# Kernel tuning notes

Hardware: AMD Instinct MI355X
Metric: run time of the kernel (lower is better)

The kernel has to match this reference:

```python
import jax, jax.numpy as jnp
import numpy as np

# Dims: img=64, Nslice=16, Ncoil=4, Nsingular=4, Necho=3, N_readout=32, Npoint=96
IMG = 64
NSLICE = 16
NCOIL = 4
NSING = 4
NECHO = 3
NRO = 32
NPT = 96


def setup_inputs() -> dict:
    key = jax.random.key(0)
    k = jax.random.split(key, 6)
    singulars = jax.random.normal(k[0], (IMG, IMG, NSLICE, NSING, NECHO, 2), jnp.float32)
    smap = jax.random.normal(k[1], (NCOIL, IMG, IMG, NSLICE, 2), jnp.float32)
    # k-space trajectory in radians, [-pi, pi)
    ktraj = (jax.random.uniform(k[2], (1, NRO, NPT, 2), jnp.float32) - 0.5) * (2.0 * np.pi)
    Ur_list = jax.random.normal(k[3], (1, NRO, NSING), jnp.float32)
    slice_bin_list = jax.random.randint(k[4], (NRO,), 0, NSLICE)
    dc = jax.random.uniform(k[5], (NPT,), jnp.float32)
    return {"singulars": singulars, "smap": smap, "ktraj": ktraj,
            "Ur_list": Ur_list, "slice_bin_list": slice_bin_list, "dc": dc}


def reference(singulars, smap, ktraj, Ur_list, slice_bin_list, dc):
    # dc is density compensation; used only in the original (custom) backward.
    X, Y, Z, Ns, Ne, _ = singulars.shape
    C = smap.shape[0]
    sc = singulars[..., 0] + 1j * singulars[..., 1]              # [X,Y,Z,Ns,Ne] c64
    sc = jnp.transpose(sc, (3, 4, 0, 1, 2)).reshape(Ns * Ne, 1, X, Y, Z)  # [S,1,X,Y,Z]
    # sign flip on odd slices (fftshift trick along kz)
    sign = jnp.where(jnp.arange(Z) % 2 == 1, -1.0, 1.0).astype(jnp.float32)
    sc = sc * sign
    sm = smap[..., 0] + 1j * smap[..., 1]                        # [C,X,Y,Z]
    sc = sc * sm[None]                                            # [S,C,X,Y,Z]
    scf = jnp.fft.fft(sc, axis=-1)                                # FFT along slice dim

    kt = ktraj[0]                                                 # [R,P,2]
    ur = Ur_list[0]                                               # [R,Ns]
    # gather the slice image for each readout
    img_g = scf[..., slice_bin_list]                              # [S,C,X,Y,R]

    xs = (jnp.arange(X) - X // 2).astype(jnp.float32)
    ys = (jnp.arange(Y) - Y // 2).astype(jnp.float32)
    # exact (type-2) NUFFT, separable phase: exp(-i(w0*x + w1*y)), centered grid
    ex = jnp.exp(-1j * kt[..., 0, None] * xs)                     # [R,P,X]
    ey = jnp.exp(-1j * kt[..., 1, None] * ys)                     # [R,P,Y]
    t1 = jnp.einsum('scxyr,rpx->scrpy', img_g, ex)                # [S,C,R,P,Y]
    nuf = jnp.einsum('scrpy,rpy->scrp', t1, ey)                   # [S,C,R,P]
    nuf = nuf.reshape(Ns, Ne, C, kt.shape[0], kt.shape[1])        # [Ns,Ne,C,R,P]
    # singular-vector weighted sum: [P,C,R,Ne]
    out = jnp.einsum('necrp,rn->pcre', nuf, ur.astype(nuf.dtype))
    # view_as_real
    return jnp.stack([out.real, out.imag], axis=-1)               # [P,C,R,Ne,2]
```

## Files before the change

### kernel.cpp

```cpp
#include <hip/hip_runtime.h>
#include <math.h>

#define IMG 64
#define NPIX 4096
#define NSLICE 16
#define NCOIL 4
#define NSING 4
#define NECHO 3
#define NRO 32
#define NPT 96
#define NEC 12

typedef float v2f __attribute__((ext_vector_type(2)));

#define EXG_F2 (NRO * IMG * NPT)

__global__ __launch_bounds__(256) void build_ex(
    const float* __restrict__ kt,
    float2* __restrict__ exg)
{
  int g = blockIdx.x * 256 + threadIdx.x;
  int p = g % 96;
  int x = (g / 96) & 63;
  int r = g / (96 * 64);
  float w0 = kt[(r * 96 + p) * 2];
  float s, c;
  __sincosf(-w0 * (float)(x - 32), &s, &c);
  exg[g] = make_float2(c, s);
}

__global__ __launch_bounds__(256) void precompute_imgw(
    const float2* __restrict__ sing,
    const float2* __restrict__ smap,
    const float*  __restrict__ ur,
    const int*    __restrict__ zb,
    float2* __restrict__ imgw)
{
  __shared__ float2 sc_sh[4 * 192];
  __shared__ float2 sm_sh[4 * 64];
  __shared__ float2 f_sh[4 * 48 * 16];
  __shared__ float  ur_sh[128];
  __shared__ int    zb_sh[32];

  const int t   = threadIdx.x;
  const int px0 = blockIdx.x * 4;

  for (int j = t; j < 768; j += 256) sc_sh[j] = sing[px0 * 192 + j];
  {
    int c = t >> 6, pxl = (t >> 4) & 3, z = t & 15;
    sm_sh[pxl * 64 + c * 16 + z] = smap[c * 65536 + (px0 + pxl) * 16 + z];
  }
  if (t < 128) ur_sh[t] = ur[t];
  if (t < 32)  zb_sh[t] = zb[t];
  __syncthreads();

  const int pxl = t >> 6, lane = t & 63;
  const int s = lane >> 2, c = lane & 3;

  const float wr[16] = { 1.f,  0.92387953f,  0.70710678f,  0.38268343f,
                         0.f, -0.38268343f, -0.70710678f, -0.92387953f,
                        -1.f, -0.92387953f, -0.70710678f, -0.38268343f,
                         0.f,  0.38268343f,  0.70710678f,  0.92387953f };
  const float wi[16] = { 0.f, -0.38268343f, -0.70710678f, -0.92387953f,
                        -1.f, -0.92387953f, -0.70710678f, -0.38268343f,
                         0.f,  0.38268343f,  0.70710678f,  0.92387953f,
                         1.f,  0.92387953f,  0.70710678f,  0.38268343f };

  if (lane < 48) {
    float br[16], bi[16];
    #pragma unroll
    for (int z = 0; z < 16; ++z) {
      float2 a = sc_sh[pxl * 192 + z * 12 + s];
      float2 m = sm_sh[pxl * 64 + c * 16 + z];
      float sg = (z & 1) ? -1.f : 1.f;
      br[z] = sg * (a.x * m.x - a.y * m.y);
      bi[z] = sg * (a.x * m.y + a.y * m.x);
    }
    float Er[8], Ei[8], Or[8], Oi[8];
    #pragma unroll
    for (int k = 0; k < 8; ++k) {
      float er = 0.f, ei = 0.f, pr = 0.f, pi = 0.f;
      #pragma unroll
      for (int m = 0; m < 8; ++m) {
        const int idx = (2 * k * m) & 15;
        er = fmaf(br[2*m],    wr[idx], er); er = fmaf(-bi[2*m],   wi[idx], er);
        ei = fmaf(br[2*m],    wi[idx], ei); ei = fmaf( bi[2*m],   wr[idx], ei);
        pr = fmaf(br[2*m+1],  wr[idx], pr); pr = fmaf(-bi[2*m+1], wi[idx], pr);
        pi = fmaf(br[2*m+1],  wi[idx], pi); pi = fmaf( bi[2*m+1], wr[idx], pi);
      }
      Er[k] = er; Ei[k] = ei; Or[k] = pr; Oi[k] = pi;
    }
    float2* frow = &f_sh[(pxl * 48 + s * 4 + c) * 16];
    #pragma unroll
    for (int k = 0; k < 8; ++k) {
      float tr = Or[k] * wr[k] - Oi[k] * wi[k];
      float ti = Or[k] * wi[k] + Oi[k] * wr[k];
      frow[k]     = make_float2(Er[k] + tr, Ei[k] + ti);
      frow[k + 8] = make_float2(Er[k] - tr, Ei[k] - ti);
    }
  }
  __syncthreads();

  for (int j = t; j < 1536; j += 256) {
    int rc  = j >> 2;
    int pl  = j & 3;
    int r   = rc / 12, ec = rc - r * 12;
    int e   = ec >> 2, cc = ec & 3;
    int kz  = zb_sh[r];
    float vr = 0.f, vi = 0.f;
    #pragma unroll
    for (int n = 0; n < 4; ++n) {
      float u  = ur_sh[r * 4 + n];
      float2 f = f_sh[(pl * 48 + (n * 3 + e) * 4 + cc) * 16 + kz];
      vr = fmaf(u, f.x, vr);
      vi = fmaf(u, f.y, vi);
    }
    imgw[rc * 4096 + px0 + pl] = make_float2(vr, vi);
  }
}

__global__ __launch_bounds__(256, 3) void nufft_points(
    const float*  __restrict__ kt,
    const float2* __restrict__ exg,
    const float2* __restrict__ imgw,
    float2* __restrict__ out)
{
  __shared__ float2 w_sh[4096];

  const int bid = blockIdx.x;
  const int r   = bid & 31;
  const int ec  = (bid >> 5) % 12;
  const int ps  = bid / 384;
  const int e   = ec >> 2, c = ec & 3;
  const int t    = threadIdx.x;
  const int lane = t & 63;
  const int p0 = __builtin_amdgcn_readfirstlane(ps * 48 + (t >> 6) * 12);

  {
    const float4* wsrc = (const float4*)(imgw + (r * 12 + ec) * 4096);
    float4* wdst = (float4*)w_sh;
    #pragma unroll
    for (int j = 0; j < 8; ++j) wdst[t + j * 256] = wsrc[t + j * 256];
  }
  __syncthreads();

  v2f accA[12], accB[12];
  #pragma unroll
  for (int pp = 0; pp < 12; ++pp) { accA[pp] = (v2f)(0.f); accB[pp] = (v2f)(0.f); }

  const v2f* __restrict__ exgv = (const v2f*)exg;

  #pragma unroll 4
  for (int x = 0; x < 64; ++x) {
    float2 w = w_sh[x * 64 + lane];
    const v2f* exb = exgv + ((r * 64 + x) * 96 + p0);
    #pragma unroll
    for (int pp = 0; pp < 12; ++pp) {
      v2f ev = exb[pp];
      v2f wx = { w.x, w.x };
      v2f wy = { w.y, w.y };
      accA[pp] = __builtin_elementwise_fma(wx, ev, accA[pp]);
      accB[pp] = __builtin_elementwise_fma(wy, ev, accB[pp]);
    }
  }

  const float yy = (float)(lane - 32);
  #pragma unroll
  for (int pp = 0; pp < 12; ++pp) {
    const int p = p0 + pp;
    float w1 = kt[(r * 96 + p) * 2 + 1];
    float es, ecos;
    __sincosf(-w1 * yy, &es, &ecos);
    float vr0 = accA[pp].x - accB[pp].y;
    float vi0 = accA[pp].y + accB[pp].x;
    float vr = vr0 * ecos - vi0 * es;
    float vi = vr0 * es + vi0 * ecos;
    #pragma unroll
    for (int off = 32; off; off >>= 1) {
      vr += __shfl_xor(vr, off);
      vi += __shfl_xor(vi, off);
    }
    if (lane == 0) out[((p * 4 + c) * 32 + r) * 3 + e] = make_float2(vr, vi);
  }
}

extern "C" void kernel_launch(void* const* d_in, const int* in_sizes, int n_in,
                              void* d_out, int out_size, void* d_ws, size_t ws_size,
                              hipStream_t stream) {
  const float2* sing  = (const float2*)d_in[0];
  const float2* smap  = (const float2*)d_in[1];
  const float*  ktraj = (const float*)d_in[2];
  const float*  ur    = (const float*)d_in[3];
  const int*    zbin  = (const int*)d_in[4];

  float2* exg  = (float2*)d_ws;
  float2* imgw = exg + EXG_F2;
  float2* out  = (float2*)d_out;

  build_ex<<<EXG_F2 / 256, 256, 0, stream>>>(ktraj, exg);
  precompute_imgw<<<NPIX / 4, 256, 0, stream>>>(sing, smap, ur, zbin, imgw);
  nufft_points<<<NRO * NEC * 2, 256, 0, stream>>>(ktraj, exg, imgw, out);
}
```

Measured before the change: 102.2 us.

## Exploit conjugate symmetry of x-phase table and fuse table build into precompute

Rewrites the x-direction NUFFT sum using exp(-i w(x-32)) symmetry: image rows at 32+k and 32-k are combined into sum and rotated difference in shared memory, so only 33 cos/sin entries per point are needed and the inner loop does half the FMAs. The separate build_ex kernel is removed and its smaller table is computed by the first blocks of precompute_imgw, saving a launch. Adds two extra shared-memory passes and barriers in nufft_points.

```diff
diff --git a/kernel.cpp b/kernel.cpp
--- a/kernel.cpp
+++ b/kernel.cpp
@@ -13,27 +13,15 @@
 
 typedef float v2f __attribute__((ext_vector_type(2)));
 
-#define EXG_F2 (NRO * IMG * NPT)
-
-__global__ __launch_bounds__(256) void build_ex(
-    const float* __restrict__ kt,
-    float2* __restrict__ exg)
-{
-  int g = blockIdx.x * 256 + threadIdx.x;
-  int p = g % 96;
-  int x = (g / 96) & 63;
-  int r = g / (96 * 64);
-  float w0 = kt[(r * 96 + p) * 2];
-  float s, c;
-  __sincosf(-w0 * (float)(x - 32), &s, &c);
-  exg[g] = make_float2(c, s);
-}
+#define EXG2_F2 (NRO * 33 * NPT)
 
 __global__ __launch_bounds__(256) void precompute_imgw(
     const float2* __restrict__ sing,
     const float2* __restrict__ smap,
     const float*  __restrict__ ur,
     const int*    __restrict__ zb,
+    const float*  __restrict__ kt,
+    float2* __restrict__ ex2,
     float2* __restrict__ imgw)
 {
   __shared__ float2 sc_sh[4 * 192];
@@ -44,6 +32,18 @@
 
   const int t   = threadIdx.x;
   const int px0 = blockIdx.x * 4;
+
+  if (blockIdx.x < 396) {
+    int g = blockIdx.x * 256 + t;
+    int p = g % 96;
+    int k = (g / 96) % 33;
+    int r = g / (96 * 33);
+    float w0 = kt[(r * 96 + p) * 2];
+    float ang = (k == 0) ? (32.0f * w0) : (-(float)k * w0);
+    float s_, c_;
+    __sincosf(ang, &s_, &c_);
+    ex2[g] = make_float2(c_, s_);
+  }
 
   for (int j = t; j < 768; j += 256) sc_sh[j] = sing[px0 * 192 + j];
   {
@@ -121,7 +121,7 @@
 
 __global__ __launch_bounds__(256, 3) void nufft_points(
     const float*  __restrict__ kt,
-    const float2* __restrict__ exg,
+    const float2* __restrict__ ex2,
     const float2* __restrict__ imgw,
     float2* __restrict__ out)
 {
@@ -144,23 +144,54 @@
   }
   __syncthreads();
 
-  v2f accA[12], accB[12];
+  float2 wa[8], wb[8];
   #pragma unroll
-  for (int pp = 0; pp < 12; ++pp) { accA[pp] = (v2f)(0.f); accB[pp] = (v2f)(0.f); }
-
-  const v2f* __restrict__ exgv = (const v2f*)exg;
-
-  #pragma unroll 4
-  for (int x = 0; x < 64; ++x) {
-    float2 w = w_sh[x * 64 + lane];
-    const v2f* exb = exgv + ((r * 64 + x) * 96 + p0);
+  for (int j = 0; j < 8; ++j) {
+    int idx = t + j * 256;
+    if (idx < 1984) {
+      int k = 1 + (idx >> 6), y = idx & 63;
+      wa[j] = w_sh[(32 + k) * 64 + y];
+      wb[j] = w_sh[(32 - k) * 64 + y];
+    }
+  }
+  __syncthreads();
+  #pragma unroll
+  for (int j = 0; j < 8; ++j) {
+    int idx = t + j * 256;
+    if (idx < 1984) {
+      int k = 1 + (idx >> 6), y = idx & 63;
+      w_sh[(32 + k) * 64 + y] = make_float2(wa[j].x + wb[j].x, wa[j].y + wb[j].y);
+      w_sh[(32 - k) * 64 + y] = make_float2(-(wa[j].y - wb[j].y), wa[j].x - wb[j].x);
+    }
+  }
+  __syncthreads();
+
+  const float* __restrict__ exb = (const float*)(ex2 + r * 33 * 96);
+
+  v2f acc[12];
+  {
+    float2 w0v = w_sh[lane];
+    float2 w32 = w_sh[32 * 64 + lane];
     #pragma unroll
     for (int pp = 0; pp < 12; ++pp) {
-      v2f ev = exb[pp];
-      v2f wx = { w.x, w.x };
-      v2f wy = { w.y, w.y };
-      accA[pp] = __builtin_elementwise_fma(wx, ev, accA[pp]);
-      accB[pp] = __builtin_elementwise_fma(wy, ev, accB[pp]);
+      float er = exb[2 * (p0 + pp)];
+      float ei = exb[2 * (p0 + pp) + 1];
+      acc[pp].x = w32.x + w0v.x * er - w0v.y * ei;
+      acc[pp].y = w32.y + w0v.x * ei + w0v.y * er;
+    }
+  }
+
+  #pragma unroll 2
+  for (int k = 1; k < 32; ++k) {
+    v2f sxy = *(const v2f*)&w_sh[(32 + k) * 64 + lane];
+    v2f dyx = *(const v2f*)&w_sh[(32 - k) * 64 + lane];
+    const float* ekb = exb + k * 192 + 2 * p0;
+    #pragma unroll
+    for (int pp = 0; pp < 12; ++pp) {
+      float er = ekb[2 * pp];
+      float ei = ekb[2 * pp + 1];
+      acc[pp] = __builtin_elementwise_fma(sxy, (v2f)(er), acc[pp]);
+      acc[pp] = __builtin_elementwise_fma(dyx, (v2f)(ei), acc[pp]);
     }
   }
 
@@ -171,10 +202,8 @@
     float w1 = kt[(r * 96 + p) * 2 + 1];
     float es, ecos;
     __sincosf(-w1 * yy, &es, &ecos);
-    float vr0 = accA[pp].x - accB[pp].y;
-    float vi0 = accA[pp].y + accB[pp].x;
-    float vr = vr0 * ecos - vi0 * es;
-    float vi = vr0 * es + vi0 * ecos;
+    float vr = acc[pp].x * ecos - acc[pp].y * es;
+    float vi = acc[pp].x * es  + acc[pp].y * ecos;
     #pragma unroll
     for (int off = 32; off; off >>= 1) {
       vr += __shfl_xor(vr, off);
@@ -193,11 +222,10 @@
   const float*  ur    = (const float*)d_in[3];
   const int*    zbin  = (const int*)d_in[4];
 
-  float2* exg  = (float2*)d_ws;
-  float2* imgw = exg + EXG_F2;
+  float2* ex2  = (float2*)d_ws;
+  float2* imgw = ex2 + EXG2_F2;
   float2* out  = (float2*)d_out;
 
-  build_ex<<<EXG_F2 / 256, 256, 0, stream>>>(ktraj, exg);
-  precompute_imgw<<<NPIX / 4, 256, 0, stream>>>(sing, smap, ur, zbin, imgw);
-  nufft_points<<<NRO * NEC * 2, 256, 0, stream>>>(ktraj, exg, imgw, out);
+  precompute_imgw<<<NPIX / 4, 256, 0, stream>>>(sing, smap, ur, zbin, ktraj, ex2, imgw);
+  nufft_points<<<NRO * NEC * 2, 256, 0, stream>>>(ktraj, ex2, imgw, out);
 }
```

Measured after the change: 99.30 us. 1.03x faster.
